# Kernel tuning notes

Measured on AMD Instinct MI355X. Metric: run time of the kernel, lower is better.

## Reference

```python
import jax, jax.numpy as jnp
import numpy as np

B, T, D_MODEL, NHEAD, D_HEAD = 8, 4096, 1024, 16, 64


def setup_inputs() -> dict:
    key = jax.random.key(0)
    ks = jax.random.split(key, 8)
    return {
        "inputs": jax.random.normal(ks[0], (B, T, D_MODEL), jnp.float32),
        "z0": jax.random.normal(ks[1], (NHEAD, D_HEAD), jnp.float32),
        "W_in": jax.random.normal(ks[2], (D_MODEL, D_MODEL), jnp.float32) / np.sqrt(D_MODEL),
        "b_in": jax.random.normal(ks[3], (D_MODEL,), jnp.float32) * 0.01,
        "W_out": jax.random.normal(ks[4], (D_MODEL, D_MODEL), jnp.float32) / np.sqrt(D_MODEL),
        "b_out": jax.random.normal(ks[5], (D_MODEL,), jnp.float32) * 0.01,
        "smoothing_logit": jax.random.normal(ks[6], (NHEAD, 1), jnp.float32),
        "v0": jax.random.normal(ks[7], (1, 1, NHEAD, D_HEAD), jnp.float32),
    }


def reference(inputs, z0, W_in, b_in, W_out, b_out, smoothing_logit, v0):
    b, t, d = inputs.shape
    nhead, d_head = z0.shape
    # in projection -> (b, t, h, d_head)
    values = (inputs @ W_in + b_in).reshape(b, t, nhead, d_head)
    # prepend learned z0, then temporal differencing -> (b, t, h, d_head)
    z0_b = jnp.broadcast_to(z0[None, None], (b, 1, nhead, d_head))
    values = jnp.concatenate([z0_b, values], axis=1)
    values = values[:, 1:] - values[:, :-1]
    # exponential smoothing recurrence: s_j = a*s_{j-1} + (1-a)*v_j, s_{-1} = v0
    alpha = jax.nn.sigmoid(smoothing_logit)           # (h, 1)
    a = alpha[None]                                   # (1, h, 1) broadcast over batch
    s0 = jnp.broadcast_to(v0[0, 0][None], (b, nhead, d_head))

    def step(s, v):                                   # v: (b, h, d_head)
        s = a * s + (1.0 - a) * v
        return s, s

    _, es_out = jax.lax.scan(step, s0, jnp.swapaxes(values, 0, 1))  # (t, b, h, d)
    es_out = jnp.swapaxes(es_out, 0, 1)               # (b, t, h, d_head)
    # prepend v0 -> length t+1
    v0_b = jnp.broadcast_to(v0, (b, 1, nhead, d_head))
    out = jnp.concatenate([v0_b, es_out], axis=1)     # (b, t+1, h, d_head)
    out = out.reshape(b, t + 1, nhead * d_head)
    return out @ W_out + b_out                        # (b, t+1, d_model)
```

## Files before the change

### kernel.cpp

```cpp
#include <hip/hip_runtime.h>
#include <hip/hip_bf16.h>
#include <stdint.h>
#include <math.h>

#define DEV static __device__ __forceinline__

typedef __attribute__((ext_vector_type(8))) short bf16x8;
typedef __attribute__((ext_vector_type(4))) float f32x4;
typedef unsigned int u32;

static constexpr int T = 4096;
static constexpr int BATCH = 8;
static constexpr int DM = 1024;
static constexpr int M1 = BATCH * T;
static constexpr int M2 = BATCH * (T + 1);
static constexpr int M2P = 129 * 256;
static constexpr int NCH = 64;
static constexpr int CL = T / NCH;
static constexpr int NT = 32;

DEV unsigned short f2bf(float f) {
  union { float f; unsigned u; } v; v.f = f;
  unsigned u = v.u;
  return (unsigned short)((u + 0x7fffu + ((u >> 16) & 1u)) >> 16);
}
DEV float bf2f(unsigned short s) {
  union { unsigned u; float f; } v; v.u = ((unsigned)s) << 16;
  return v.f;
}

DEV void gl_lds16(const unsigned short* g, unsigned short* lds) {
  __builtin_amdgcn_global_load_lds(
      (const __attribute__((address_space(1))) u32*)g,
      (__attribute__((address_space(3))) u32*)lds,
      16, 0, 0);
}

__global__ void k_cvt_x(const float4* __restrict__ x, ushort4* __restrict__ o) {
  int i = blockIdx.x * 256 + threadIdx.x;
  float4 v = x[i];
  ushort4 r;
  r.x = f2bf(v.x); r.y = f2bf(v.y); r.z = f2bf(v.z); r.w = f2bf(v.w);
  o[i] = r;
}

__global__ void k_transpose(const float* __restrict__ w0, const float* __restrict__ w1,
                            unsigned short* __restrict__ t0, unsigned short* __restrict__ t1) {
  __shared__ float tile[32][33];
  const float* src = blockIdx.z ? w1 : w0;
  unsigned short* dst = blockIdx.z ? t1 : t0;
  int bx = blockIdx.x * 32;
  int by = blockIdx.y * 32;
  int tx = threadIdx.x & 31, ty = threadIdx.x >> 5;
#pragma unroll
  for (int r = 0; r < 32; r += 8)
    tile[ty + r][tx] = src[(by + ty + r) * DM + bx + tx];
  __syncthreads();
#pragma unroll
  for (int r = 0; r < 32; r += 8)
    dst[(bx + ty + r) * DM + by + tx] = f2bf(tile[tx][ty + r]);
}

template <int MODE>
__global__ __launch_bounds__(512, 4) void k_gemm(const unsigned short* __restrict__ A16,
                                                 const unsigned short* __restrict__ Bt16,
                                                 const float* __restrict__ bias,
                                                 unsigned short* __restrict__ outb,
                                                 float* __restrict__ outf, int Mvalid,
                                                 const float* __restrict__ slog,
                                                 float* __restrict__ chunkL,
                                                 float* __restrict__ plastg) {
  __shared__ unsigned short lds[24576];

  const int tid = threadIdx.x;
  const int w = tid >> 6, l = tid & 63;
  const int wm = w >> 1, wn = w & 1;
  const int lo = l & 15, hi = l >> 4;

  const int nwg = gridDim.x, orig = blockIdx.x;
  const int cpx = nwg >> 3;
  const int wg = (orig & 7) * cpx + (orig >> 3);
  const int bm = wg >> 3, bn = wg & 7;
  const int blockM = bm * 256;
  const int blockN = bn * 128;

  f32x4 acc[4][4];
#pragma unroll
  for (int m = 0; m < 4; m++)
#pragma unroll
    for (int n = 0; n < 4; n++) acc[m][n] = (f32x4){0.f, 0.f, 0.f, 0.f};

  const int sg = (l & 3) ^ ((l >> 3) & 3);
  const unsigned short* pA[2];
#pragma unroll
  for (int c = 0; c < 2; c++)
    pA[c] = A16 + (size_t)(blockM + w * 32 + c * 16 + (l >> 2)) * DM + sg * 8;
  const unsigned short* pB =
      Bt16 + (size_t)(blockN + w * 16 + (l >> 2)) * DM + sg * 8;

  auto stage = [&](int tt, int buf) {
#pragma unroll
    for (int c = 0; c < 2; c++)
      gl_lds16(pA[c] + (size_t)tt * 32, &lds[buf * 12288 + (w * 32 + c * 16) * 32]);
    gl_lds16(pB + (size_t)tt * 32, &lds[buf * 12288 + 8192 + (w * 16) * 32]);
  };

  stage(0, 0);
  __syncthreads();

  for (int t = 0; t < NT; ++t) {
    const int cur = t & 1;
    if (t + 1 < NT) stage(t + 1, cur ^ 1);

    bf16x8 aq[4], bq[4];
#pragma unroll
    for (int mf = 0; mf < 4; mf++) {
      const int r = wm * 64 + mf * 16 + lo;
      aq[mf] = *(const bf16x8*)(&lds[cur * 12288 + r * 32 + (hi ^ ((r >> 1) & 3)) * 8]);
    }
#pragma unroll
    for (int nf = 0; nf < 4; nf++) {
      const int r = wn * 64 + nf * 16 + lo;
      bq[nf] = *(const bf16x8*)(&lds[cur * 12288 + 8192 + r * 32 + (hi ^ ((r >> 1) & 3)) * 8]);
    }
#pragma unroll
    for (int mf = 0; mf < 4; mf++)
#pragma unroll
      for (int nf = 0; nf < 4; nf++)
        acc[mf][nf] = __builtin_amdgcn_mfma_f32_16x16x32_bf16(
            bq[nf], aq[mf], acc[mf][nf], 0, 0, 0);

    __syncthreads();
  }

#pragma unroll
  for (int mf = 0; mf < 4; mf++) {
    const int row = blockM + wm * 64 + mf * 16 + lo;
    if (MODE == 1 && row >= Mvalid) continue;
#pragma unroll
    for (int nf = 0; nf < 4; nf++) {
      const int col = blockN + wn * 64 + nf * 16 + hi * 4;
      const float4 bv = *(const float4*)(bias + col);
      if (MODE == 0) {
        ushort4 o;
        o.x = f2bf(acc[mf][nf][0] + bv.x);
        o.y = f2bf(acc[mf][nf][1] + bv.y);
        o.z = f2bf(acc[mf][nf][2] + bv.z);
        o.w = f2bf(acc[mf][nf][3] + bv.w);
        *(ushort4*)(outb + (size_t)row * DM + col) = o;
      } else {
        float4 o;
        o.x = acc[mf][nf][0] + bv.x;
        o.y = acc[mf][nf][1] + bv.y;
        o.z = acc[mf][nf][2] + bv.z;
        o.w = acc[mf][nf][3] + bv.w;
        *(float4*)(outf + (size_t)row * DM + col) = o;
      }
    }
  }

  if (MODE == 0) {
    const float aa = 1.f / (1.f + expf(-slog[(blockN + wn * 64) >> 6]));
    const float one_a = 1.f - aa;
    const float a2v = aa * aa, a4v = a2v * a2v, a8v = a4v * a4v, a16v = a8v * a8v;
    const float w3raw = powf(aa, (float)(14 - lo));
    float wv[4];
    wv[3] = (lo == 15) ? 0.f : w3raw;
    wv[2] = w3raw * a16v;
    wv[1] = wv[2] * a16v;
    wv[0] = wv[1] * a16v;
    float S[4][4], P63[4][4];
#pragma unroll
    for (int nf = 0; nf < 4; nf++) {
      const int col = blockN + wn * 64 + nf * 16 + hi * 4;
      const float4 bv = *(const float4*)(bias + col);
#pragma unroll
      for (int j = 0; j < 4; j++) {
        const float bj = ((const float*)&bv)[j];
        float s = 0.f, p63 = 0.f;
#pragma unroll
        for (int mf = 0; mf < 4; mf++) {
          const float p = acc[mf][nf][j] + bj;
          s += wv[mf] * p;
          if (mf == 3 && lo == 15) p63 = p;
        }
        S[nf][j] = s;
        P63[nf][j] = p63;
      }
    }
#pragma unroll
    for (int nf = 0; nf < 4; nf++)
#pragma unroll
      for (int j = 0; j < 4; j++)
#pragma unroll
        for (int m = 1; m < 16; m <<= 1) {
          S[nf][j] += __shfl_xor(S[nf][j], m);
          P63[nf][j] += __shfl_xor(P63[nf][j], m);
        }
    const int cglob = (blockM >> 6) + wm;
    if (lo == 0 || lo == 1) {
#pragma unroll
      for (int nf = 0; nf < 4; nf++)
#pragma unroll
        for (int j = 0; j < 4; j++) {
          const int col = blockN + wn * 64 + nf * 16 + hi * 4 + j;
          if (lo == 0)
            chunkL[(size_t)cglob * DM + col] =
                one_a * P63[nf][j] - one_a * one_a * S[nf][j];
          else
            plastg[(size_t)cglob * DM + col] = P63[nf][j];
        }
    }
  }
}

__global__ void k_scan_combine(const float* __restrict__ chunkL,
                               const float* __restrict__ plastg,
                               const float* __restrict__ logit,
                               const float* __restrict__ z0,
                               const float* __restrict__ v0,
                               float* __restrict__ enter) {
  const int b = blockIdx.x;
  const int ch0 = threadIdx.x * 4;
  const float a = 1.f / (1.f + expf(-logit[ch0 >> 6]));
  const float a2 = a * a, a4 = a2 * a2, a8 = a4 * a4, a16 = a8 * a8, a32 = a16 * a16;
  const float aL = a32 * a32;
  const float g = (1.f - a) * a32 * a16 * a8 * a4 * a2 * a;
  float4 e = *(const float4*)(v0 + ch0);
  float4 pp = *(const float4*)(z0 + ch0);
  *(float4*)(enter + (size_t)(b * NCH) * DM + ch0) = e;
  for (int c = 1; c < NCH; c++) {
    const float4 L = *(const float4*)(chunkL + (size_t)(b * NCH + c - 1) * DM + ch0);
    e.x = aL * e.x + (L.x - g * pp.x);
    e.y = aL * e.y + (L.y - g * pp.y);
    e.z = aL * e.z + (L.z - g * pp.z);
    e.w = aL * e.w + (L.w - g * pp.w);
    *(float4*)(enter + (size_t)(b * NCH + c) * DM + ch0) = e;
    pp = *(const float4*)(plastg + (size_t)(b * NCH + c - 1) * DM + ch0);
  }
}

__global__ void k_scan_final(const unsigned short* __restrict__ proj,
                             const float* __restrict__ logit,
                             const float* __restrict__ z0,
                             const float* __restrict__ v0,
                             const float* __restrict__ enter,
                             unsigned short* __restrict__ S) {
  const int b = blockIdx.x >> 6, c = blockIdx.x & 63;
  const int ch0 = threadIdx.x * 8;
  const float a = 1.f / (1.f + expf(-logit[ch0 >> 6]));
  const int t0 = c * CL;
  const unsigned short* p = proj + (size_t)(b * T + t0) * DM + ch0;
  unsigned short* so = S + (size_t)(b * (T + 1) + t0 + 1) * DM + ch0;
  float pprev[8], s[8];
  if (t0 == 0) {
#pragma unroll
    for (int k = 0; k < 8; k++) pprev[k] = z0[ch0 + k];
  } else {
    bf16x8 v = *(const bf16x8*)(p - DM);
#pragma unroll
    for (int k = 0; k < 8; k++) pprev[k] = bf2f((unsigned short)v[k]);
  }
  {
    const float* e = enter + (size_t)(b * NCH + c) * DM + ch0;
#pragma unroll
    for (int k = 0; k < 8; k++) s[k] = e[k];
  }
  if (c == 0) {
    bf16x8 r;
#pragma unroll
    for (int k = 0; k < 8; k++) r[k] = (short)f2bf(v0[ch0 + k]);
    *(bf16x8*)(S + (size_t)b * (T + 1) * DM + ch0) = r;
  }
  for (int j = 0; j < CL; j++) {
    bf16x8 v = *(const bf16x8*)(p + (size_t)j * DM);
    bf16x8 r;
#pragma unroll
    for (int k = 0; k < 8; k++) {
      float pv = bf2f((unsigned short)v[k]);
      s[k] = a * s[k] + (1.f - a) * (pv - pprev[k]);
      pprev[k] = pv;
      r[k] = (short)f2bf(s[k]);
    }
    *(bf16x8*)(so + (size_t)j * DM) = r;
  }
}

extern "C" void kernel_launch(void* const* d_in, const int* in_sizes, int n_in,
                              void* d_out, int out_size, void* d_ws, size_t ws_size,
                              hipStream_t stream) {
  const float* inputs = (const float*)d_in[0];
  const float* z0     = (const float*)d_in[1];
  const float* W_in   = (const float*)d_in[2];
  const float* b_in   = (const float*)d_in[3];
  const float* W_out  = (const float*)d_in[4];
  const float* b_out  = (const float*)d_in[5];
  const float* slogit = (const float*)d_in[6];
  const float* v0     = (const float*)d_in[7];
  float* out = (float*)d_out;

  char* ws = (char*)d_ws;
  unsigned short* X16   = (unsigned short*)(ws);
  unsigned short* P16   = (unsigned short*)(ws + 67108864);
  unsigned short* S16   = (unsigned short*)(ws + 134217728);
  unsigned short* WTin  = (unsigned short*)(ws + 201850880);
  unsigned short* WTout = (unsigned short*)(ws + 203948032);
  float* chunkend       = (float*)(ws + 206045184);
  float* enter          = (float*)(ws + 208142336);
  float* plast          = (float*)(ws + 210239488);

  k_cvt_x<<<32768, 256, 0, stream>>>((const float4*)inputs, (ushort4*)X16);
  k_transpose<<<dim3(32, 32, 2), 256, 0, stream>>>(W_in, W_out, WTin, WTout);
  k_gemm<0><<<dim3((M1 / 256) * 8), 512, 0, stream>>>(X16, WTin, b_in, P16, nullptr, M1,
                                                      slogit, chunkend, plast);
  k_scan_combine<<<dim3(BATCH), 256, 0, stream>>>(chunkend, plast, slogit, z0, v0, enter);
  k_scan_final<<<dim3(BATCH * NCH), 128, 0, stream>>>(P16, slogit, z0, v0, enter, S16);
  k_gemm<1><<<dim3((M2P / 256) * 8), 512, 0, stream>>>(S16, WTout, b_out, nullptr, out, M2,
                                                       nullptr, nullptr, nullptr);
}
```

Before: 279.5 us.

## Fuse fp32-to-bf16 input conversion into first GEMM's A-tile load

Drops the separate conversion kernel that wrote a bf16 copy of the inputs. The first GEMM now stages fp32 A tiles straight into LDS with an XOR swizzle and converts them to bf16 in registers before each MFMA. This removes a full extra read and write pass over the activations. In exchange it doubles the A bytes loaded per tile, grows LDS per block (which may cut occupancy), and repeats the conversion work across every column block.

After: 289.5 us. +3.6%, slower.

```diff
diff --git a/kernel.cpp b/kernel.cpp
--- a/kernel.cpp
+++ b/kernel.cpp
@@ -18,6 +18,7 @@
 static constexpr int NCH = 64;
 static constexpr int CL = T / NCH;
 static constexpr int NT = 32;
+static constexpr int BUFB = 40960;
 
 DEV unsigned short f2bf(float f) {
   union { float f; unsigned u; } v; v.f = f;
@@ -29,19 +30,11 @@
   return v.f;
 }
 
-DEV void gl_lds16(const unsigned short* g, unsigned short* lds) {
+DEV void gl_lds16(const void* g, void* lds) {
   __builtin_amdgcn_global_load_lds(
       (const __attribute__((address_space(1))) u32*)g,
       (__attribute__((address_space(3))) u32*)lds,
       16, 0, 0);
-}
-
-__global__ void k_cvt_x(const float4* __restrict__ x, ushort4* __restrict__ o) {
-  int i = blockIdx.x * 256 + threadIdx.x;
-  float4 v = x[i];
-  ushort4 r;
-  r.x = f2bf(v.x); r.y = f2bf(v.y); r.z = f2bf(v.z); r.w = f2bf(v.w);
-  o[i] = r;
 }
 
 __global__ void k_transpose(const float* __restrict__ w0, const float* __restrict__ w1,
@@ -62,7 +55,7 @@
 }
 
 template <int MODE>
-__global__ __launch_bounds__(512, 4) void k_gemm(const unsigned short* __restrict__ A16,
+__global__ __launch_bounds__(512, 4) void k_gemm(const void* __restrict__ Asrc,
                                                  const unsigned short* __restrict__ Bt16,
                                                  const float* __restrict__ bias,
                                                  unsigned short* __restrict__ outb,
@@ -70,7 +63,7 @@
                                                  const float* __restrict__ slog,
                                                  float* __restrict__ chunkL,
                                                  float* __restrict__ plastg) {
-  __shared__ unsigned short lds[24576];
+  __shared__ char smem[2 * BUFB];
 
   const int tid = threadIdx.x;
   const int w = tid >> 6, l = tid & 63;
@@ -84,25 +77,44 @@
   const int blockM = bm * 256;
   const int blockN = bn * 128;
 
+  const float* A32 = (const float*)Asrc;
+  const unsigned short* A16 = (const unsigned short*)Asrc;
+
   f32x4 acc[4][4];
 #pragma unroll
   for (int m = 0; m < 4; m++)
 #pragma unroll
     for (int n = 0; n < 4; n++) acc[m][n] = (f32x4){0.f, 0.f, 0.f, 0.f};
 
-  const int sg = (l & 3) ^ ((l >> 3) & 3);
-  const unsigned short* pA[2];
-#pragma unroll
-  for (int c = 0; c < 2; c++)
-    pA[c] = A16 + (size_t)(blockM + w * 32 + c * 16 + (l >> 2)) * DM + sg * 8;
+  const int sgB = (l & 3) ^ ((l >> 3) & 3);
   const unsigned short* pB =
-      Bt16 + (size_t)(blockN + w * 16 + (l >> 2)) * DM + sg * 8;
+      Bt16 + (size_t)(blockN + w * 16 + (l >> 2)) * DM + sgB * 8;
+
+  const int sgA0 = (l & 7) ^ ((l >> 3) & 7);
+  const float* pA32[4];
+  const unsigned short* pA16[2];
+  if (MODE == 0) {
+#pragma unroll
+    for (int c = 0; c < 4; c++)
+      pA32[c] = A32 + (size_t)(blockM + c * 64 + w * 8 + (l >> 3)) * DM + sgA0 * 4;
+  } else {
+#pragma unroll
+    for (int c = 0; c < 2; c++)
+      pA16[c] = A16 + (size_t)(blockM + w * 32 + c * 16 + (l >> 2)) * DM + sgB * 8;
+  }
 
   auto stage = [&](int tt, int buf) {
-#pragma unroll
-    for (int c = 0; c < 2; c++)
-      gl_lds16(pA[c] + (size_t)tt * 32, &lds[buf * 12288 + (w * 32 + c * 16) * 32]);
-    gl_lds16(pB + (size_t)tt * 32, &lds[buf * 12288 + 8192 + (w * 16) * 32]);
+    char* base = smem + buf * BUFB;
+    if (MODE == 0) {
+#pragma unroll
+      for (int c = 0; c < 4; c++)
+        gl_lds16(pA32[c] + (size_t)tt * 32, base + (c * 64 + w * 8) * 128);
+    } else {
+#pragma unroll
+      for (int c = 0; c < 2; c++)
+        gl_lds16(pA16[c] + (size_t)tt * 32, base + (w * 32 + c * 16) * 64);
+    }
+    gl_lds16(pB + (size_t)tt * 32, base + 32768 + (w * 16) * 64);
   };
 
   stage(0, 0);
@@ -113,15 +125,38 @@
     if (t + 1 < NT) stage(t + 1, cur ^ 1);
 
     bf16x8 aq[4], bq[4];
-#pragma unroll
-    for (int mf = 0; mf < 4; mf++) {
-      const int r = wm * 64 + mf * 16 + lo;
-      aq[mf] = *(const bf16x8*)(&lds[cur * 12288 + r * 32 + (hi ^ ((r >> 1) & 3)) * 8]);
-    }
-#pragma unroll
-    for (int nf = 0; nf < 4; nf++) {
-      const int r = wn * 64 + nf * 16 + lo;
-      bq[nf] = *(const bf16x8*)(&lds[cur * 12288 + 8192 + r * 32 + (hi ^ ((r >> 1) & 3)) * 8]);
+    if (MODE == 0) {
+      const float* La = (const float*)(smem + cur * BUFB);
+#pragma unroll
+      for (int mf = 0; mf < 4; mf++) {
+        const int r = wm * 64 + mf * 16 + lo;
+        const int s0 = (2 * hi) ^ (r & 7);
+        const int s1 = (2 * hi + 1) ^ (r & 7);
+        const f32x4 x0 = *(const f32x4*)(La + r * 32 + s0 * 4);
+        const f32x4 x1 = *(const f32x4*)(La + r * 32 + s1 * 4);
+        bf16x8 a;
+#pragma unroll
+        for (int k = 0; k < 4; k++) {
+          a[k] = (short)f2bf(x0[k]);
+          a[4 + k] = (short)f2bf(x1[k]);
+        }
+        aq[mf] = a;
+      }
+    } else {
+      const unsigned short* La = (const unsigned short*)(smem + cur * BUFB);
+#pragma unroll
+      for (int mf = 0; mf < 4; mf++) {
+        const int r = wm * 64 + mf * 16 + lo;
+        aq[mf] = *(const bf16x8*)(La + r * 32 + (hi ^ ((r >> 1) & 3)) * 8);
+      }
+    }
+    {
+      const unsigned short* Lb = (const unsigned short*)(smem + cur * BUFB + 32768);
+#pragma unroll
+      for (int nf = 0; nf < 4; nf++) {
+        const int r = wn * 64 + nf * 16 + lo;
+        bq[nf] = *(const bf16x8*)(Lb + r * 32 + (hi ^ ((r >> 1) & 3)) * 8);
+      }
     }
 #pragma unroll
     for (int mf = 0; mf < 4; mf++)
@@ -300,18 +335,16 @@
   float* out = (float*)d_out;
 
   char* ws = (char*)d_ws;
-  unsigned short* X16   = (unsigned short*)(ws);
-  unsigned short* P16   = (unsigned short*)(ws + 67108864);
-  unsigned short* S16   = (unsigned short*)(ws + 134217728);
-  unsigned short* WTin  = (unsigned short*)(ws + 201850880);
-  unsigned short* WTout = (unsigned short*)(ws + 203948032);
-  float* chunkend       = (float*)(ws + 206045184);
-  float* enter          = (float*)(ws + 208142336);
-  float* plast          = (float*)(ws + 210239488);
-
-  k_cvt_x<<<32768, 256, 0, stream>>>((const float4*)inputs, (ushort4*)X16);
+  unsigned short* P16   = (unsigned short*)(ws);
+  unsigned short* S16   = (unsigned short*)(ws + 67108864);
+  unsigned short* WTin  = (unsigned short*)(ws + 134742016);
+  unsigned short* WTout = (unsigned short*)(ws + 136839168);
+  float* chunkend       = (float*)(ws + 138936320);
+  float* enter          = (float*)(ws + 141033472);
+  float* plast          = (float*)(ws + 143130624);
+
   k_transpose<<<dim3(32, 32, 2), 256, 0, stream>>>(W_in, W_out, WTin, WTout);
-  k_gemm<0><<<dim3((M1 / 256) * 8), 512, 0, stream>>>(X16, WTin, b_in, P16, nullptr, M1,
+  k_gemm<0><<<dim3((M1 / 256) * 8), 512, 0, stream>>>(inputs, WTin, b_in, P16, nullptr, M1,
                                                       slogit, chunkend, plast);
   k_scan_combine<<<dim3(BATCH), 256, 0, stream>>>(chunkend, plast, slogit, z0, v0, enter);
   k_scan_final<<<dim3(BATCH * NCH), 128, 0, stream>>>(P16, slogit, z0, v0, enter, S16);
```
